# Performance work log

Hardware: AMD Instinct MI355X
Metric: run time of the kernel (lower is better)

Reference implementation:

```python
import jax, jax.numpy as jnp
import numpy as np

B, S, D, H = 16, 4096, 768, 12  # batch, seqlen, dim, num_heads
KS = 9  # res_kernel_size


def setup_inputs() -> dict:
    key = jax.random.key(0)
    ks = jax.random.split(key, 6)
    x = jax.random.normal(ks[0], (B, S, D), dtype=jnp.float32)
    w_qkv = jax.random.normal(ks[1], (3 * D, D), dtype=jnp.float32) * 0.02
    b_qkv = jax.random.normal(ks[2], (3 * D,), dtype=jnp.float32) * 0.02
    w_proj = jax.random.normal(ks[3], (D, D), dtype=jnp.float32) * 0.02
    b_proj = jax.random.normal(ks[4], (D,), dtype=jnp.float32) * 0.02
    # depthwise conv over (seq, head_dim) spatial dims: kernel (KS, 1), groups=H
    w_dconv = jax.random.normal(ks[5], (H, 1, KS, 1), dtype=jnp.float32) * 0.1
    return {"x": x, "w_qkv": w_qkv, "b_qkv": b_qkv,
            "w_proj": w_proj, "b_proj": b_proj, "w_dconv": w_dconv}


def reference(x, w_qkv, b_qkv, w_proj, b_proj, w_dconv):
    Bz, Sz, Dz = x.shape
    Hh = w_dconv.shape[0]
    d = Dz // Hh  # head_dim
    # qkv projection: [B,S,3D] -> [3,B,H,S,d]  (rearrange 's (n h d) -> n h s d')
    qkv = jnp.einsum('bsd,ed->bse', x, w_qkv) + b_qkv
    qkv = qkv.reshape(Bz, Sz, 3, Hh, d).transpose(2, 0, 3, 1, 4)
    q, k, v = qkv[0], qkv[1], qkv[2]  # each [B,H,S,d]
    # L2-normalize q, k along head dim
    q = q / jnp.linalg.norm(q, axis=-1, keepdims=True)
    k = k / jnp.linalg.norm(k, axis=-1, keepdims=True)
    # depthwise conv on v: NCHW = [B, H, S, d], kernel (KS,1), pad (KS//2, 0)
    pad = w_dconv.shape[2] // 2
    dconv_v = jax.lax.conv_general_dilated(
        v, w_dconv, window_strides=(1, 1),
        padding=((pad, pad), (0, 0)), feature_group_count=Hh)
    # linear angular attention: kv = k^T v  ([B,H,d,d]), then q @ kv
    kv = jnp.einsum('bhsd,bhse->bhde', k, v)
    out = 0.5 * v + (1.0 / jnp.pi) * jnp.einsum('bhsd,bhde->bhse', q, kv)
    out = out / jnp.linalg.norm(out, axis=-1, keepdims=True)
    out = out + dconv_v
    # 'h s d -> s (h d)' (with batch): [B,H,S,d] -> [B,S,H*d]
    out = out.transpose(0, 2, 1, 3).reshape(Bz, Sz, Dz)
    return jnp.einsum('bsd,ed->bse', out, w_proj) + b_proj
```

## Files before the change

kernel.cpp:

```cpp
#include <hip/hip_runtime.h>
#include <hip/hip_bf16.h>

#define DEV __device__ __forceinline__

typedef __attribute__((ext_vector_type(8))) short bf16x8;
typedef __attribute__((ext_vector_type(4))) float f32x4;

DEV unsigned short bfbits(float x) {
    __hip_bfloat16 b = __float2bfloat16(x);
    return __builtin_bit_cast(unsigned short, b);
}
DEV float b2f(unsigned short u) {
    __hip_bfloat16 b = __builtin_bit_cast(__hip_bfloat16, u);
    return __bfloat162float(b);
}

DEV void gl2lds16(const void* g, void* l) {
    __builtin_amdgcn_global_load_lds(
        (const __attribute__((address_space(1))) void*)g,
        (__attribute__((address_space(3))) void*)l,
        16, 0, 0);
}

#define WAIT_VM4()  asm volatile("s_waitcnt vmcnt(4)" ::: "memory")
#define WAIT_VM0()  asm volatile("s_waitcnt vmcnt(0)" ::: "memory")
#define BARRIER()   asm volatile("s_barrier"          ::: "memory")

__global__ __launch_bounds__(256) void cvt_bf16(const float* __restrict__ in,
                                                unsigned short* __restrict__ out, int n) {
    int i = (blockIdx.x * 256 + threadIdx.x) * 4;
    if (i >= n) return;
    float4 f = *(const float4*)(in + i);
    ushort4 u;
    u.x = bfbits(f.x); u.y = bfbits(f.y); u.z = bfbits(f.z); u.w = bfbits(f.w);
    *(ushort4*)(out + i) = u;
}

template <int EPI>
__global__ __launch_bounds__(512, 2) void gemm256(
        const unsigned short* __restrict__ A,
        const unsigned short* __restrict__ B,
        const float* __restrict__ bias,
        float* __restrict__ Cf,
        unsigned short* __restrict__ qhat,
        unsigned short* __restrict__ khat,
        unsigned short* __restrict__ varr,
        int N) {
    constexpr int K = 768, NT = 12;
    __shared__ __align__(16) unsigned short sh[65536];
    const int t = threadIdx.x;
    const int wave = t >> 6, lane = t & 63;
    const int quad = lane >> 4, l16 = lane & 15;
    const int wm = wave >> 2, wn = wave & 3;

    const int gx = gridDim.x;
    const int nwg = gx * gridDim.y;
    const int wg0 = blockIdx.y * gx + blockIdx.x;
    const int swz = (wg0 & 7) * (nwg >> 3) + (wg0 >> 3);
    const int m0 = (swz / gx) * 256;
    const int n0 = (swz % gx) * 256;

    const unsigned short* Abase = A + (size_t)m0 * K;
    const unsigned short* Bbase = B + (size_t)n0 * K;

    const int scb = (t & 3) ^ ((t >> 3) & 3);
    const size_t soff = (size_t)(t >> 2) * K + scb * 8;
    auto STAGE = [&](const unsigned short* g, unsigned short* l) {
        gl2lds16(g + soff, l + t * 8);
        gl2lds16(g + soff + 128 * K, l + 4096 + t * 8);
    };

    const int cb8 = (quad ^ ((l16 >> 1) & 3)) * 8;
    const int aoff = (wm * 128 + l16) * 32 + cb8;
    const int boff = (wn * 64 + l16) * 32 + cb8;

    STAGE(Abase,      sh);
    STAGE(Bbase,      sh + 16384);
    STAGE(Abase + 32, sh + 8192);
    STAGE(Bbase + 32, sh + 24576);

    f32x4 acc[8][4] = {};

#pragma unroll 2
    for (int kt = 0; kt < NT; ++kt) {
        unsigned short* buf  = sh + (kt & 1) * 32768;
        unsigned short* nbuf = sh + ((kt + 1) & 1) * 32768;
        const unsigned short* An = Abase + (kt + 1) * 64;
        const unsigned short* Bn = Bbase + (kt + 1) * 64;
        bf16x8 afr[4], bfr[4];

        WAIT_VM4();
        BARRIER();
#pragma unroll
        for (int i = 0; i < 4; i++) afr[i] = *(const bf16x8*)(buf + aoff + i * 512);
#pragma unroll
        for (int j = 0; j < 4; j++) bfr[j] = *(const bf16x8*)(buf + 16384 + boff + j * 512);
        if (kt + 1 < NT) STAGE(An, nbuf);
        __builtin_amdgcn_s_setprio(1);
#pragma unroll
        for (int i = 0; i < 4; i++)
#pragma unroll
            for (int j = 0; j < 4; j++)
                acc[i][j] = __builtin_amdgcn_mfma_f32_16x16x32_bf16(afr[i], bfr[j], acc[i][j], 0, 0, 0);
        __builtin_amdgcn_s_setprio(0);

#pragma unroll
        for (int i = 0; i < 4; i++) afr[i] = *(const bf16x8*)(buf + aoff + (i + 4) * 512);
        if (kt + 1 < NT) STAGE(Bn, nbuf + 16384);
        __builtin_amdgcn_s_setprio(1);
#pragma unroll
        for (int i = 0; i < 4; i++)
#pragma unroll
            for (int j = 0; j < 4; j++)
                acc[i + 4][j] = __builtin_amdgcn_mfma_f32_16x16x32_bf16(afr[i], bfr[j], acc[i + 4][j], 0, 0, 0);
        __builtin_amdgcn_s_setprio(0);

        if (kt + 1 < NT) { WAIT_VM4(); } else { WAIT_VM0(); }
        BARRIER();
#pragma unroll
        for (int i = 0; i < 4; i++) afr[i] = *(const bf16x8*)(buf + 8192 + aoff + i * 512);
#pragma unroll
        for (int j = 0; j < 4; j++) bfr[j] = *(const bf16x8*)(buf + 24576 + boff + j * 512);
        if (kt + 1 < NT) STAGE(An + 32, nbuf + 8192);
        __builtin_amdgcn_s_setprio(1);
#pragma unroll
        for (int i = 0; i < 4; i++)
#pragma unroll
            for (int j = 0; j < 4; j++)
                acc[i][j] = __builtin_amdgcn_mfma_f32_16x16x32_bf16(afr[i], bfr[j], acc[i][j], 0, 0, 0);
        __builtin_amdgcn_s_setprio(0);

#pragma unroll
        for (int i = 0; i < 4; i++) afr[i] = *(const bf16x8*)(buf + 8192 + aoff + (i + 4) * 512);
        if (kt + 1 < NT) STAGE(Bn + 32, nbuf + 24576);
        __builtin_amdgcn_s_setprio(1);
#pragma unroll
        for (int i = 0; i < 4; i++)
#pragma unroll
            for (int j = 0; j < 4; j++)
                acc[i + 4][j] = __builtin_amdgcn_mfma_f32_16x16x32_bf16(afr[i], bfr[j], acc[i + 4][j], 0, 0, 0);
        __builtin_amdgcn_s_setprio(0);
    }

    const int colbase = n0 + wn * 64;
    if constexpr (EPI == 0) {
#pragma unroll
        for (int j = 0; j < 4; j++) {
            int col = colbase + j * 16 + l16;
            float bv = bias[col];
#pragma unroll
            for (int i = 0; i < 8; i++)
#pragma unroll
                for (int r = 0; r < 4; r++) {
                    int row = m0 + wm * 128 + i * 16 + quad * 4 + r;
                    Cf[(size_t)row * N + col] = acc[i][j][r] + bv;
                }
        }
    } else {
        const int sec = colbase / 768;
        const int cin = colbase - sec * 768;
        const int h = cin >> 6;
        const int b = m0 >> 12;
        unsigned short* dst = (sec == 0) ? qhat : (sec == 1) ? khat : varr;
        const size_t headbase = (size_t)(b * 12 + h) * 4096;
        float bv[4];
#pragma unroll
        for (int j = 0; j < 4; j++) bv[j] = bias[colbase + j * 16 + l16];
#pragma unroll
        for (int i = 0; i < 8; i++) {
            float o[4][4];
#pragma unroll
            for (int j = 0; j < 4; j++)
#pragma unroll
                for (int r = 0; r < 4; r++) o[j][r] = acc[i][j][r] + bv[j];
            if (sec < 2) {
#pragma unroll
                for (int r = 0; r < 4; r++) {
                    float ss = o[0][r]*o[0][r] + o[1][r]*o[1][r] + o[2][r]*o[2][r] + o[3][r]*o[3][r];
                    ss += __shfl_xor(ss, 1, 64);
                    ss += __shfl_xor(ss, 2, 64);
                    ss += __shfl_xor(ss, 4, 64);
                    ss += __shfl_xor(ss, 8, 64);
                    float sc = rsqrtf(ss);
#pragma unroll
                    for (int j = 0; j < 4; j++) o[j][r] *= sc;
                }
            }
#pragma unroll
            for (int j = 0; j < 4; j++)
#pragma unroll
                for (int r = 0; r < 4; r++) {
                    int s = (m0 + wm * 128 + i * 16 + quad * 4 + r) & 4095;
                    dst[(headbase + s) * 64 + j * 16 + l16] = bfbits(o[j][r]);
                }
        }
    }
}

__global__ __launch_bounds__(256) void kv_kernel(const unsigned short* __restrict__ khat,
                                                 const unsigned short* __restrict__ varr,
                                                 float* __restrict__ kvpart) {
    const int bh = blockIdx.x >> 2, chunk = blockIdx.x & 3;
    const int t = threadIdx.x, wave = t >> 6, lane = t & 63;
    __shared__ __align__(16) float kt[64 * 64];
    __shared__ __align__(16) float vt[64 * 64];
    const int e0 = (lane >> 3) * 8, f0 = (lane & 7) * 8;
    float acc[8][8] = {};

    for (int tile = 0; tile < 16; tile++) {
        int sbase = chunk * 1024 + tile * 64;
        __syncthreads();
#pragma unroll
        for (int i = 0; i < 2; i++) {
            int c = t + i * 256;
            int row = c >> 3, off = (c & 7) * 8;
            size_t g = ((size_t)bh * 4096 + sbase + row) * 64 + off;
            bf16x8 kk = *(const bf16x8*)(khat + g);
            bf16x8 vv = *(const bf16x8*)(varr + g);
#pragma unroll
            for (int j = 0; j < 8; j++) {
                kt[row * 64 + off + j] = b2f((unsigned short)kk[j]);
                vt[row * 64 + off + j] = b2f((unsigned short)vv[j]);
            }
        }
        __syncthreads();
#pragma unroll
        for (int dsi = 0; dsi < 16; dsi++) {
            int ds = wave * 16 + dsi;
            f32x4 ka = *(f32x4*)&kt[ds * 64 + e0], kb = *(f32x4*)&kt[ds * 64 + e0 + 4];
            f32x4 va = *(f32x4*)&vt[ds * 64 + f0], vb = *(f32x4*)&vt[ds * 64 + f0 + 4];
            float ke[8] = {ka.x, ka.y, ka.z, ka.w, kb.x, kb.y, kb.z, kb.w};
            float vf[8] = {va.x, va.y, va.z, va.w, vb.x, vb.y, vb.z, vb.w};
#pragma unroll
            for (int i = 0; i < 8; i++)
#pragma unroll
                for (int j = 0; j < 8; j++) acc[i][j] += ke[i] * vf[j];
        }
    }
    __syncthreads();
    float* red = kt;
    for (int w = 0; w < 4; w++) {
        if (wave == w) {
#pragma unroll
            for (int i = 0; i < 8; i++)
#pragma unroll
                for (int j = 0; j < 8; j++) {
                    int idx = (e0 + i) * 64 + f0 + j;
                    if (w == 0) red[idx] = acc[i][j];
                    else        red[idx] += acc[i][j];
                }
        }
        __syncthreads();
    }
    float* outp = kvpart + (size_t)blockIdx.x * 4096;
#pragma unroll
    for (int i = 0; i < 16; i++) outp[t + i * 256] = red[t + i * 256];
}

__global__ __launch_bounds__(256) void kvred_kernel(const float* __restrict__ kvpart,
                                                    unsigned short* __restrict__ kvT) {
    const int bh = blockIdx.x;
    const int t = threadIdx.x;
    __shared__ float kvf[64 * 65];
    const float* p0 = kvpart + (size_t)(bh * 4) * 4096;
#pragma unroll
    for (int i = 0; i < 16; i++) {
        int idx = t + i * 256;
        int e = idx >> 6, f = idx & 63;
        kvf[e * 65 + f] = p0[idx] + p0[4096 + idx] + p0[8192 + idx] + p0[12288 + idx];
    }
    __syncthreads();
#pragma unroll
    for (int i = 0; i < 16; i++) {
        int o = t + i * 256;
        int f = o >> 6, e = o & 63;
        kvT[(size_t)bh * 4096 + o] = bfbits(kvf[e * 65 + f]);
    }
}

__global__ __launch_bounds__(256) void attn_kernel(const unsigned short* __restrict__ qhat,
                                                   const unsigned short* __restrict__ varr,
                                                   const unsigned short* __restrict__ kvT,
                                                   const float* __restrict__ wdconv,
                                                   __hip_bfloat16* __restrict__ outpre) {
    const int st = blockIdx.x;
    const int bh = blockIdx.y;
    const int b = bh / 12, h = bh % 12;
    const int s0 = st * 128;
    const int t = threadIdx.x, w = t >> 6, lane = t & 63;
    const int quad = lane >> 4, l16 = lane & 15;

    __shared__ __align__(16) unsigned short vt[136 * 64];
    __shared__ float oL[128 * 65];

    const size_t vb = (size_t)bh * 4096;
#pragma unroll
    for (int i = 0; i < 5; i++) {
        int c = t + i * 256;
        if (c < 1088) {
            int row = c >> 3, off = (c & 7) * 8;
            int gs = s0 - 4 + row;
            bf16x8 vv = {};
            if ((unsigned)gs < 4096u) vv = *(const bf16x8*)(varr + (vb + gs) * 64 + off);
            *(bf16x8*)&vt[row * 64 + off] = vv;
        }
    }

    bf16x8 bfr[2][4];
#pragma unroll
    for (int ks = 0; ks < 2; ks++)
#pragma unroll
        for (int j = 0; j < 4; j++)
            bfr[ks][j] = *(const bf16x8*)(kvT + (size_t)bh * 4096 + (j * 16 + l16) * 64 + ks * 32 + quad * 8);

    f32x4 acc[2][4] = {};
#pragma unroll
    for (int i = 0; i < 2; i++) {
#pragma unroll
        for (int ks = 0; ks < 2; ks++) {
            bf16x8 af = *(const bf16x8*)(qhat + (vb + s0 + w * 32 + i * 16 + l16) * 64 + ks * 32 + quad * 8);
#pragma unroll
            for (int j = 0; j < 4; j++)
                acc[i][j] = __builtin_amdgcn_mfma_f32_16x16x32_bf16(af, bfr[ks][j], acc[i][j], 0, 0, 0);
        }
    }
    __syncthreads();

    const float inv_pi = 0.3183098861837907f;
#pragma unroll
    for (int i = 0; i < 2; i++) {
        float o[4][4];
#pragma unroll
        for (int r = 0; r < 4; r++) {
            int rl = w * 32 + i * 16 + quad * 4 + r;
#pragma unroll
            for (int j = 0; j < 4; j++) {
                float vval = b2f(vt[(rl + 4) * 64 + j * 16 + l16]);
                o[j][r] = 0.5f * vval + inv_pi * acc[i][j][r];
            }
            float ss = o[0][r]*o[0][r] + o[1][r]*o[1][r] + o[2][r]*o[2][r] + o[3][r]*o[3][r];
            ss += __shfl_xor(ss, 1, 64);
            ss += __shfl_xor(ss, 2, 64);
            ss += __shfl_xor(ss, 4, 64);
            ss += __shfl_xor(ss, 8, 64);
            float sc = rsqrtf(ss);
#pragma unroll
            for (int j = 0; j < 4; j++)
                oL[rl * 65 + j * 16 + l16] = o[j][r] * sc;
        }
    }
    __syncthreads();

    float wc[9];
#pragma unroll
    for (int j = 0; j < 9; j++) wc[j] = wdconv[h * 9 + j];
#pragma unroll
    for (int i = 0; i < 32; i++) {
        int c = t + i * 256;
        int sl = c >> 6, f = c & 63;
        float cc = 0.f;
#pragma unroll
        for (int j = 0; j < 9; j++) cc += wc[j] * b2f(vt[(sl + j) * 64 + f]);
        float oo = oL[sl * 65 + f] + cc;
        outpre[(size_t)(b * 4096 + s0 + sl) * 768 + h * 64 + f] = __float2bfloat16(oo);
    }
}

extern "C" void kernel_launch(void* const* d_in, const int* in_sizes, int n_in,
                              void* d_out, int out_size, void* d_ws, size_t ws_size,
                              hipStream_t stream) {
    const float* x      = (const float*)d_in[0];
    const float* w_qkv  = (const float*)d_in[1];
    const float* b_qkv  = (const float*)d_in[2];
    const float* w_proj = (const float*)d_in[3];
    const float* b_proj = (const float*)d_in[4];
    const float* w_dc   = (const float*)d_in[5];
    float* out = (float*)d_out;

    char* ws = (char*)d_ws;
    unsigned short* xb      = (unsigned short*)(ws + 0);
    unsigned short* wqkvb   = (unsigned short*)(ws + 100663296);
    unsigned short* wprojb  = (unsigned short*)(ws + 104202240);
    unsigned short* qhat    = (unsigned short*)(ws + 105381888);
    unsigned short* khat    = (unsigned short*)(ws + 206045184);
    unsigned short* varr    = (unsigned short*)(ws + 306708480);
    float* kvpart           = (float*)(ws + 407371776);
    unsigned short* kvT     = (unsigned short*)(ws + 419954688);

    const int NX = 16 * 4096 * 768;
    const int NWQ = 2304 * 768;
    const int NWP = 768 * 768;

    cvt_bf16<<<NX / 1024, 256, 0, stream>>>(x, xb, NX);
    cvt_bf16<<<NWQ / 1024, 256, 0, stream>>>(w_qkv, wqkvb, NWQ);
    cvt_bf16<<<NWP / 1024, 256, 0, stream>>>(w_proj, wprojb, NWP);

    gemm256<1><<<dim3(2304 / 256, 65536 / 256), 512, 0, stream>>>(
        xb, wqkvb, b_qkv, nullptr, qhat, khat, varr, 2304);

    kv_kernel<<<192 * 4, 256, 0, stream>>>(khat, varr, kvpart);

    kvred_kernel<<<192, 256, 0, stream>>>(kvpart, kvT);

    attn_kernel<<<dim3(32, 192), 256, 0, stream>>>(qhat, varr, kvT, w_dc, (__hip_bfloat16*)xb);

    gemm256<0><<<dim3(768 / 256, 65536 / 256), 512, 0, stream>>>(
        xb, wprojb, b_proj, out, nullptr, nullptr, nullptr, 768);
}
```

Measured before the change: 877.4 us.

## Restructure GEMM main loop into 4-stage LDS ring with 3-deep prefetch

Replaces the double-buffered two-half-tile scheme with a four-slot LDS ring of 32-wide K sub-tiles. Three sub-tiles are prefetched ahead and the wait uses vmcnt(8). There is now one barrier per sub-tile, and the loop is fully unrolled over 24 steps. The aim is to hide global-to-LDS load latency better behind MFMA work. In exchange it adds more outstanding loads, a longer unrolled body and a barrier per 32-K step, which may raise instruction-cache and register pressure.

```diff
diff --git a/kernel.cpp b/kernel.cpp
--- a/kernel.cpp
+++ b/kernel.cpp
@@ -22,6 +22,7 @@
         16, 0, 0);
 }
 
+#define WAIT_VM8()  asm volatile("s_waitcnt vmcnt(8)" ::: "memory")
 #define WAIT_VM4()  asm volatile("s_waitcnt vmcnt(4)" ::: "memory")
 #define WAIT_VM0()  asm volatile("s_waitcnt vmcnt(0)" ::: "memory")
 #define BARRIER()   asm volatile("s_barrier"          ::: "memory")
@@ -46,7 +47,7 @@
         unsigned short* __restrict__ khat,
         unsigned short* __restrict__ varr,
         int N) {
-    constexpr int K = 768, NT = 12;
+    constexpr int K = 768, NU = 24;
     __shared__ __align__(16) unsigned short sh[65536];
     const int t = threadIdx.x;
     const int wave = t >> 6, lane = t & 63;
@@ -65,37 +66,37 @@
 
     const int scb = (t & 3) ^ ((t >> 3) & 3);
     const size_t soff = (size_t)(t >> 2) * K + scb * 8;
-    auto STAGE = [&](const unsigned short* g, unsigned short* l) {
-        gl2lds16(g + soff, l + t * 8);
-        gl2lds16(g + soff + 128 * K, l + 4096 + t * 8);
+    auto STAGEU = [&](int u) {
+        unsigned short* l = sh + (u & 3) * 16384;
+        const unsigned short* ga = Abase + (u >> 1) * 64 + (u & 1) * 32;
+        const unsigned short* gb = Bbase + (u >> 1) * 64 + (u & 1) * 32;
+        gl2lds16(ga + soff,           l + t * 8);
+        gl2lds16(ga + soff + 128 * K, l + 4096 + t * 8);
+        gl2lds16(gb + soff,           l + 8192 + t * 8);
+        gl2lds16(gb + soff + 128 * K, l + 12288 + t * 8);
     };
 
     const int cb8 = (quad ^ ((l16 >> 1) & 3)) * 8;
     const int aoff = (wm * 128 + l16) * 32 + cb8;
     const int boff = (wn * 64 + l16) * 32 + cb8;
 
-    STAGE(Abase,      sh);
-    STAGE(Bbase,      sh + 16384);
-    STAGE(Abase + 32, sh + 8192);
-    STAGE(Bbase + 32, sh + 24576);
+    STAGEU(0); STAGEU(1); STAGEU(2);
 
     f32x4 acc[8][4] = {};
 
-#pragma unroll 2
-    for (int kt = 0; kt < NT; ++kt) {
-        unsigned short* buf  = sh + (kt & 1) * 32768;
-        unsigned short* nbuf = sh + ((kt + 1) & 1) * 32768;
-        const unsigned short* An = Abase + (kt + 1) * 64;
-        const unsigned short* Bn = Bbase + (kt + 1) * 64;
+#pragma unroll
+    for (int u = 0; u < NU; ++u) {
+        if (u < NU - 2)      { WAIT_VM8(); }
+        else if (u == NU - 2){ WAIT_VM4(); }
+        else                 { WAIT_VM0(); }
+        BARRIER();
+        const unsigned short* buf = sh + (u & 3) * 16384;
         bf16x8 afr[4], bfr[4];
-
-        WAIT_VM4();
-        BARRIER();
+#pragma unroll
+        for (int j = 0; j < 4; j++) bfr[j] = *(const bf16x8*)(buf + 8192 + boff + j * 512);
 #pragma unroll
         for (int i = 0; i < 4; i++) afr[i] = *(const bf16x8*)(buf + aoff + i * 512);
-#pragma unroll
-        for (int j = 0; j < 4; j++) bfr[j] = *(const bf16x8*)(buf + 16384 + boff + j * 512);
-        if (kt + 1 < NT) STAGE(An, nbuf);
+        if (u + 3 < NU) STAGEU(u + 3);
         __builtin_amdgcn_s_setprio(1);
 #pragma unroll
         for (int i = 0; i < 4; i++)
@@ -103,36 +104,8 @@
             for (int j = 0; j < 4; j++)
                 acc[i][j] = __builtin_amdgcn_mfma_f32_16x16x32_bf16(afr[i], bfr[j], acc[i][j], 0, 0, 0);
         __builtin_amdgcn_s_setprio(0);
-
 #pragma unroll
         for (int i = 0; i < 4; i++) afr[i] = *(const bf16x8*)(buf + aoff + (i + 4) * 512);
-        if (kt + 1 < NT) STAGE(Bn, nbuf + 16384);
-        __builtin_amdgcn_s_setprio(1);
-#pragma unroll
-        for (int i = 0; i < 4; i++)
-#pragma unroll
-            for (int j = 0; j < 4; j++)
-                acc[i + 4][j] = __builtin_amdgcn_mfma_f32_16x16x32_bf16(afr[i], bfr[j], acc[i + 4][j], 0, 0, 0);
-        __builtin_amdgcn_s_setprio(0);
-
-        if (kt + 1 < NT) { WAIT_VM4(); } else { WAIT_VM0(); }
-        BARRIER();
-#pragma unroll
-        for (int i = 0; i < 4; i++) afr[i] = *(const bf16x8*)(buf + 8192 + aoff + i * 512);
-#pragma unroll
-        for (int j = 0; j < 4; j++) bfr[j] = *(const bf16x8*)(buf + 24576 + boff + j * 512);
-        if (kt + 1 < NT) STAGE(An + 32, nbuf + 8192);
-        __builtin_amdgcn_s_setprio(1);
-#pragma unroll
-        for (int i = 0; i < 4; i++)
-#pragma unroll
-            for (int j = 0; j < 4; j++)
-                acc[i][j] = __builtin_amdgcn_mfma_f32_16x16x32_bf16(afr[i], bfr[j], acc[i][j], 0, 0, 0);
-        __builtin_amdgcn_s_setprio(0);
-
-#pragma unroll
-        for (int i = 0; i < 4; i++) afr[i] = *(const bf16x8*)(buf + 8192 + aoff + (i + 4) * 512);
-        if (kt + 1 < NT) STAGE(Bn + 32, nbuf + 24576);
         __builtin_amdgcn_s_setprio(1);
 #pragma unroll
         for (int i = 0; i < 4; i++)
```

Measured after the change: 899.7 us. 2.5% more time.
